# Optimization experiments

Hardware: AMD Instinct MI355X
Metric: run time of the kernel (lower is better)

The kernel has to match this reference:

```python
import jax, jax.numpy as jnp
import numpy as np

N = 50000      # nodes
F = 128        # num_features
E = 1600000    # edges
NHID = 256
J = 3          # orders
L = 3          # layers
G = 512        # graphs in batch
C = 10         # num_classes
NUM_DIFF = 13  # 1 + J + J^2


def setup_inputs() -> dict:
    key = jax.random.key(0)
    ks = jax.random.split(key, 32)
    rn = lambda k, shape, s=0.05: (jax.random.normal(k, shape, jnp.float32) * s)
    inp = {}
    inp["x"] = jax.random.normal(ks[0], (N, F), jnp.float32)
    inp["edge_index"] = jax.random.randint(ks[1], (2, E), 0, N)
    inp["diff_feat"] = jax.random.normal(ks[2], (NUM_DIFF, N, F), jnp.float32)
    inp["batch"] = jnp.sort(jax.random.randint(ks[3], (N,), 0, G))
    conv_in = [F, 2 * NHID, 2 * NHID]
    lin_in = [F * (J ** i) for i in range(L)]
    k = 4
    for i in range(L):
        inp[f"W_conv{i}"] = rn(ks[k], (conv_in[i], NHID)); k += 1
        inp[f"b_conv{i}"] = rn(ks[k], (NHID,)); k += 1
        inp[f"W_lin{i}"] = rn(ks[k], (lin_in[i], NHID)); k += 1
        inp[f"b_lin{i}"] = rn(ks[k], (NHID,)); k += 1
    bound = 1.0 / np.sqrt(J)
    inp["order_weights"] = jax.random.uniform(ks[k], (J,), jnp.float32, -bound, bound); k += 1
    inp["W_cls"] = rn(ks[k], (2 * NHID, NHID)); k += 1
    inp["b_cls"] = rn(ks[k], (NHID,)); k += 1
    inp["W_fc"] = rn(ks[k], (NHID, C)); k += 1
    inp["b_fc"] = rn(ks[k], (C,)); k += 1
    return inp


def _forward(x, diff_feat, order_weights, convW, convB, linW, linB,
             W_cls, b_cls, W_fc, b_fc, edge_index, batch):
    # GCNConv normalization with self-loops: D^-1/2 (A+I) D^-1/2
    loop = jnp.arange(N)
    src = jnp.concatenate([edge_index[0], loop])
    dst = jnp.concatenate([edge_index[1], loop])
    deg = jax.ops.segment_sum(jnp.ones((src.shape[0],), x.dtype), dst, num_segments=N)
    dinv = deg ** -0.5  # deg >= 1 due to self loops
    norm = (dinv[src] * dinv[dst])[:, None]

    def gcn(h, W, b):
        h = h @ W
        return jax.ops.segment_sum(h[src] * norm, dst, num_segments=N) + b

    comb = x
    begin = 0
    for i in range(L):
        convx = jax.nn.relu(gcn(comb, convW[i], convB[i]))  # dropout = identity (eval)
        count = J ** i
        lf = diff_feat[begin:begin + count]  # [count, N, F]
        if i > 0:
            ow = jnp.tile(order_weights, J ** (i - 1))[:, None, None]
            lf = ow * lf
        lf = jnp.moveaxis(lf, 0, 1).reshape(N, -1)  # [N, count*F]
        lin_sct = jax.nn.relu(lf @ linW[i] + linB[i])
        comb = jnp.concatenate([lin_sct, convx], axis=-1)  # [N, 2*NHID]
        begin += count
    convx = gcn(comb, W_cls, b_cls)  # no relu on final conv
    h_pooled = jax.ops.segment_sum(convx, batch, num_segments=G)  # global_add_pool
    return h_pooled @ W_fc + b_fc  # [G, C]


def reference(x, edge_index, diff_feat, batch,
              W_conv0, b_conv0, W_conv1, b_conv1, W_conv2, b_conv2,
              W_lin0, b_lin0, W_lin1, b_lin1, W_lin2, b_lin2,
              order_weights, W_cls, b_cls, W_fc, b_fc):
    convW = [W_conv0, W_conv1, W_conv2]
    convB = [b_conv0, b_conv1, b_conv2]
    linW = [W_lin0, W_lin1, W_lin2]
    linB = [b_lin0, b_lin1, b_lin2]
    return _forward(x, diff_feat, order_weights, convW, convB, linW, linB,
                    W_cls, b_cls, W_fc, b_fc, edge_index, batch)
```

## Files before the change

### kernel.cpp

```cpp
#include <hip/hip_runtime.h>

namespace {
constexpr int NN  = 50000;
constexpr int FF  = 128;
constexpr int EE  = 1600000;
constexpr int HID = 256;
constexpr int GG  = 512;
constexpr int CC  = 10;
}


__global__ __launch_bounds__(256) void k_zero_out(float* p, int n) {
    int i = blockIdx.x * 256 + threadIdx.x;
    if (i < n) p[i] = 0.0f;
}

__global__ __launch_bounds__(256) void k_fill_int(int* p, int val, int n) {
    int i = blockIdx.x * 256 + threadIdx.x;
    if (i < n) p[i] = val;
}

__global__ __launch_bounds__(256) void k_count(const int* __restrict__ dst,
                                               int* __restrict__ deg, int n) {
    int i = blockIdx.x * 256 + threadIdx.x;
    if (i < n) atomicAdd(&deg[dst[i]], 1);
}

__global__ __launch_bounds__(256) void k_dinv(const int* __restrict__ deg,
                                              float* __restrict__ dinv, int n) {
    int i = blockIdx.x * 256 + threadIdx.x;
    if (i < n) dinv[i] = 1.0f / sqrtf((float)deg[i]);
}

__global__ __launch_bounds__(256) void k_scan1(const int* __restrict__ deg,
                                               int* __restrict__ rowstart,
                                               int* __restrict__ bsum, int n) {
    __shared__ int s[256];
    int tid = threadIdx.x;
    int i = blockIdx.x * 256 + tid;
    int v = (i < n) ? (deg[i] - 1) : 0;
    s[tid] = v;
    __syncthreads();
    for (int off = 1; off < 256; off <<= 1) {
        int t = (tid >= off) ? s[tid - off] : 0;
        __syncthreads();
        s[tid] += t;
        __syncthreads();
    }
    if (i < n) rowstart[i] = s[tid] - v;
    if (tid == 255) bsum[blockIdx.x] = s[255];
}

__global__ __launch_bounds__(256) void k_scan2(int* __restrict__ bsum, int nb) {
    __shared__ int s[256];
    int tid = threadIdx.x;
    int v = (tid < nb) ? bsum[tid] : 0;
    s[tid] = v;
    __syncthreads();
    for (int off = 1; off < 256; off <<= 1) {
        int t = (tid >= off) ? s[tid - off] : 0;
        __syncthreads();
        s[tid] += t;
        __syncthreads();
    }
    if (tid < nb) bsum[tid] = s[tid] - v;
}

__global__ __launch_bounds__(256) void k_scan3(int* __restrict__ rowstart,
                                               const int* __restrict__ bsum,
                                               int n, int total) {
    int i = blockIdx.x * 256 + threadIdx.x;
    if (i < n) rowstart[i] += bsum[blockIdx.x];
    if (i == 0) rowstart[n] = total;
}

__global__ __launch_bounds__(256) void k_copy_int(const int* __restrict__ a,
                                                  int* __restrict__ b, int n) {
    int i = blockIdx.x * 256 + threadIdx.x;
    if (i < n) b[i] = a[i];
}

__global__ __launch_bounds__(256) void k_scatter(const int* __restrict__ srcs,
                                                 const int* __restrict__ dsts,
                                                 const float* __restrict__ dinv,
                                                 int* __restrict__ cursor,
                                                 int* __restrict__ csr_src,
                                                 float* __restrict__ csr_norm, int n) {
    int e = blockIdx.x * 256 + threadIdx.x;
    if (e < n) {
        int s = srcs[e], d = dsts[e];
        int pos = atomicAdd(&cursor[d], 1);
        csr_src[pos]  = s;
        csr_norm[pos] = dinv[s] * dinv[d];
    }
}

__global__ __launch_bounds__(256) void k_scale_wlin(const float* __restrict__ W,
                                                    const float* __restrict__ ow,
                                                    float* __restrict__ out, int total) {
    int i = blockIdx.x * 256 + threadIdx.x;
    if (i < total) {
        int row = i >> 8;
        out[i] = W[i] * ow[(row >> 7) % 3];
    }
}

__global__ __launch_bounds__(256) void k_gbounds(const int* __restrict__ batch,
                                                 int* __restrict__ gstart, int n, int g) {
    int i = blockIdx.x * 256 + threadIdx.x;
    if (i >= n) return;
    int b = batch[i];
    if (i == 0) {
        for (int q = 0; q <= b; ++q) gstart[q] = 0;
    } else {
        int bp = batch[i - 1];
        for (int q = bp + 1; q <= b; ++q) gstart[q] = i;
    }
    if (i == n - 1) {
        for (int q = b + 1; q <= g; ++q) gstart[q] = n;
    }
}

template <int VEC> struct VecT;
template <> struct VecT<4> { using T = float4; };
template <> struct VecT<2> { using T = float2; };

template <int VEC>
__global__ __launch_bounds__(256) void k_agg(const float* __restrict__ H,
                                             const int* __restrict__ rowstart,
                                             const int* __restrict__ csr_src,
                                             const float* __restrict__ csr_norm,
                                             const float* __restrict__ dinv,
                                             const float* __restrict__ bias,
                                             float* __restrict__ out,
                                             int out_stride, int out_off,
                                             int do_relu, int nN) {
    using VT = typename VecT<VEC>::T;
    constexpr int WIDTH = 64 * VEC;
    int n = (blockIdx.x * blockDim.x + threadIdx.x) >> 6;
    int lane = threadIdx.x & 63;
    if (n >= nN) return;

    float di = dinv[n];
    float selfw = di * di;
    float acc[VEC];
    {
        VT v = *reinterpret_cast<const VT*>(H + (size_t)n * WIDTH + lane * VEC);
        const float* vf = reinterpret_cast<const float*>(&v);
#pragma unroll
        for (int j = 0; j < VEC; ++j) acc[j] = vf[j] * selfw;
    }
    int s = rowstart[n], e = rowstart[n + 1];
    int i = s;
    for (; i + 3 < e; i += 4) {
        int s0 = csr_src[i], s1 = csr_src[i + 1], s2 = csr_src[i + 2], s3 = csr_src[i + 3];
        float w0 = csr_norm[i], w1 = csr_norm[i + 1], w2 = csr_norm[i + 2], w3 = csr_norm[i + 3];
        VT v0 = *reinterpret_cast<const VT*>(H + (size_t)s0 * WIDTH + lane * VEC);
        VT v1 = *reinterpret_cast<const VT*>(H + (size_t)s1 * WIDTH + lane * VEC);
        VT v2 = *reinterpret_cast<const VT*>(H + (size_t)s2 * WIDTH + lane * VEC);
        VT v3 = *reinterpret_cast<const VT*>(H + (size_t)s3 * WIDTH + lane * VEC);
        const float* f0 = reinterpret_cast<const float*>(&v0);
        const float* f1 = reinterpret_cast<const float*>(&v1);
        const float* f2 = reinterpret_cast<const float*>(&v2);
        const float* f3 = reinterpret_cast<const float*>(&v3);
#pragma unroll
        for (int j = 0; j < VEC; ++j)
            acc[j] += f0[j] * w0 + f1[j] * w1 + f2[j] * w2 + f3[j] * w3;
    }
    for (; i < e; ++i) {
        int ss = csr_src[i];
        float w = csr_norm[i];
        VT v = *reinterpret_cast<const VT*>(H + (size_t)ss * WIDTH + lane * VEC);
        const float* vf = reinterpret_cast<const float*>(&v);
#pragma unroll
        for (int j = 0; j < VEC; ++j) acc[j] += vf[j] * w;
    }
    if (bias) {
#pragma unroll
        for (int j = 0; j < VEC; ++j) acc[j] += bias[lane * VEC + j];
    }
    if (do_relu) {
#pragma unroll
        for (int j = 0; j < VEC; ++j) acc[j] = fmaxf(acc[j], 0.0f);
    }
    VT o;
    float* of = reinterpret_cast<float*>(&o);
#pragma unroll
    for (int j = 0; j < VEC; ++j) of[j] = acc[j];
    *reinterpret_cast<VT*>(out + (size_t)n * out_stride + out_off + lane * VEC) = o;
}

template <int LAYOUT>
__global__ __launch_bounds__(256) void k_gemm(const float* __restrict__ A, int ldaOrPlane,
                                              const float* __restrict__ W,
                                              const float* __restrict__ bias,
                                              float* __restrict__ out,
                                              int out_stride, int out_off,
                                              int nRows, int K, int do_relu) {
    __shared__ float As[16 * 132];
    __shared__ float Ws[16 * 64];
    int tid = threadIdx.x;
    int m0 = blockIdx.x * 128;
    int n0 = blockIdx.y * 64;
    int tx = tid & 15;
    int ty = tid >> 4;

    float acc[8][4];
#pragma unroll
    for (int i = 0; i < 8; ++i)
#pragma unroll
        for (int j = 0; j < 4; ++j) acc[i][j] = 0.0f;

    int nTiles = K >> 4;
    for (int t = 0; t < nTiles; ++t) {
        int k0 = t << 4;
        const float* Atile;
        int alda;
        if (LAYOUT == 0) {
            Atile = A + k0;
            alda = ldaOrPlane;
        } else {
            Atile = A + (size_t)(k0 >> 7) * ldaOrPlane + (k0 & 127);
            alda = 128;
        }
#pragma unroll
        for (int p = 0; p < 2; ++p) {
            int idx = tid + p * 256;
            int r = idx >> 2;
            int kk4 = idx & 3;
            float4 v = make_float4(0.f, 0.f, 0.f, 0.f);
            if (m0 + r < nRows)
                v = *reinterpret_cast<const float4*>(Atile + (size_t)(m0 + r) * alda + kk4 * 4);
            As[(kk4 * 4 + 0) * 132 + r] = v.x;
            As[(kk4 * 4 + 1) * 132 + r] = v.y;
            As[(kk4 * 4 + 2) * 132 + r] = v.z;
            As[(kk4 * 4 + 3) * 132 + r] = v.w;
        }
        {
            int kk = tid >> 4;
            int nn4 = tid & 15;
            float4 v = *reinterpret_cast<const float4*>(W + (size_t)(k0 + kk) * 256 + n0 + nn4 * 4);
            *reinterpret_cast<float4*>(Ws + kk * 64 + nn4 * 4) = v;
        }
        __syncthreads();
#pragma unroll
        for (int kk = 0; kk < 16; ++kk) {
            float4 a0 = *reinterpret_cast<const float4*>(As + kk * 132 + ty * 8);
            float4 a1 = *reinterpret_cast<const float4*>(As + kk * 132 + ty * 8 + 4);
            float4 w  = *reinterpret_cast<const float4*>(Ws + kk * 64 + tx * 4);
            float av[8] = {a0.x, a0.y, a0.z, a0.w, a1.x, a1.y, a1.z, a1.w};
            float wv[4] = {w.x, w.y, w.z, w.w};
#pragma unroll
            for (int i = 0; i < 8; ++i)
#pragma unroll
                for (int j = 0; j < 4; ++j) acc[i][j] += av[i] * wv[j];
        }
        __syncthreads();
    }
    float bv[4] = {0.f, 0.f, 0.f, 0.f};
    if (bias) {
#pragma unroll
        for (int j = 0; j < 4; ++j) bv[j] = bias[n0 + tx * 4 + j];
    }
#pragma unroll
    for (int i = 0; i < 8; ++i) {
        int gm = m0 + ty * 8 + i;
        if (gm < nRows) {
            float4 v;
            float r0 = acc[i][0] + bv[0];
            float r1 = acc[i][1] + bv[1];
            float r2 = acc[i][2] + bv[2];
            float r3 = acc[i][3] + bv[3];
            if (do_relu) {
                r0 = fmaxf(r0, 0.f); r1 = fmaxf(r1, 0.f);
                r2 = fmaxf(r2, 0.f); r3 = fmaxf(r3, 0.f);
            }
            v.x = r0; v.y = r1; v.z = r2; v.w = r3;
            *reinterpret_cast<float4*>(out + (size_t)gm * out_stride + out_off + n0 + tx * 4) = v;
        }
    }
}


__global__ __launch_bounds__(256) void k_pool(const float* __restrict__ Cfin,
                                              const int* __restrict__ gstart,
                                              float* __restrict__ pooled) {
    int g = blockIdx.x;
    int f = threadIdx.x;
    float acc = 0.0f;
    int s = gstart[g], e = gstart[g + 1];
    for (int n = s; n < e; ++n) acc += Cfin[(size_t)n * 512 + f];
    pooled[g * 256 + f] = acc;
}

__global__ __launch_bounds__(64) void k_fc(const float* __restrict__ pooled,
                                           const float* __restrict__ Wfc,
                                           const float* __restrict__ bfc,
                                           float* __restrict__ outp) {
    __shared__ float h[256];
    int g = blockIdx.x;
    for (int k = threadIdx.x; k < 256; k += 64) h[k] = pooled[g * 256 + k];
    __syncthreads();
    int c = threadIdx.x;
    if (c < CC) {
        float a = bfc[c];
        for (int k = 0; k < 256; ++k) a += h[k] * Wfc[k * CC + c];
        outp[g * CC + c] = a;
    }
}


extern "C" void kernel_launch(void* const* d_in, const int* in_sizes, int n_in,
                              void* d_out, int out_size, void* d_ws, size_t ws_size,
                              hipStream_t stream) {
    const float* x         = (const float*)d_in[0];
    const int*   edge      = (const int*)d_in[1];
    const float* diff_feat = (const float*)d_in[2];
    const int*   batch     = (const int*)d_in[3];
    const float* W_conv0 = (const float*)d_in[4];
    const float* b_conv0 = (const float*)d_in[5];
    const float* W_lin0  = (const float*)d_in[6];
    const float* b_lin0  = (const float*)d_in[7];
    const float* W_conv1 = (const float*)d_in[8];
    const float* b_conv1 = (const float*)d_in[9];
    const float* W_lin1  = (const float*)d_in[10];
    const float* b_lin1  = (const float*)d_in[11];
    const float* W_conv2 = (const float*)d_in[12];
    const float* b_conv2 = (const float*)d_in[13];
    const float* W_lin2  = (const float*)d_in[14];
    const float* b_lin2  = (const float*)d_in[15];
    const float* order_w = (const float*)d_in[16];
    const float* W_cls   = (const float*)d_in[17];
    const float* b_cls   = (const float*)d_in[18];
    const float* W_fc    = (const float*)d_in[19];
    const float* b_fc    = (const float*)d_in[20];
    float* outp = (float*)d_out;

    const int* esrc = edge;
    const int* edst = edge + EE;

    char* w = (char*)d_ws;
    size_t off = 0;
    auto alloc = [&](size_t bytes) {
        void* p = w + off;
        off = (off + bytes + 255) & ~(size_t)255;
        return p;
    };
    float* comb     = (float*)alloc((size_t)NN * 512 * 4);
    float* Bbuf     = (float*)alloc((size_t)NN * 256 * 4);
    float* Tbuf     = Bbuf;
    int*   csr_src  = (int*)alloc((size_t)EE * 4);
    float* csr_norm = (float*)alloc((size_t)EE * 4);
    int*   degi     = (int*)alloc((size_t)NN * 4);
    float* dinv     = (float*)alloc((size_t)NN * 4);
    int*   rowstart = (int*)alloc((size_t)(NN + 1) * 4);
    int*   cursor   = (int*)alloc((size_t)NN * 4);
    int*   bsum     = (int*)alloc(256 * 4);
    float* wlin1s   = (float*)alloc((size_t)384 * 256 * 4);
    float* wlin2s   = (float*)alloc((size_t)1152 * 256 * 4);
    int*   gstart   = (int*)alloc((size_t)(GG + 1) * 4);
    float* pooled   = (float*)alloc((size_t)GG * 256 * 4);
    (void)n_in; (void)in_sizes;

    if (ws_size < off) {
        k_zero_out<<<(out_size + 255) / 256, 256, 0, stream>>>(outp, out_size);
        return;
    }

    const int NB_N = (NN + 255) / 256;
    const int NB_E = (EE + 255) / 256;

    k_fill_int<<<NB_N, 256, 0, stream>>>(degi, 1, NN);
    k_count<<<NB_E, 256, 0, stream>>>(edst, degi, EE);
    k_dinv<<<NB_N, 256, 0, stream>>>(degi, dinv, NN);
    k_scan1<<<NB_N, 256, 0, stream>>>(degi, rowstart, bsum, NN);
    k_scan2<<<1, 256, 0, stream>>>(bsum, NB_N);
    k_scan3<<<NB_N, 256, 0, stream>>>(rowstart, bsum, NN, EE);
    k_copy_int<<<NB_N, 256, 0, stream>>>(rowstart, cursor, NN);
    k_scatter<<<NB_E, 256, 0, stream>>>(esrc, edst, dinv, cursor, csr_src, csr_norm, EE);
    k_scale_wlin<<<(384 * 256) / 256, 256, 0, stream>>>(W_lin1, order_w, wlin1s, 384 * 256);
    k_scale_wlin<<<(1152 * 256) / 256, 256, 0, stream>>>(W_lin2, order_w, wlin2s, 1152 * 256);
    k_gbounds<<<NB_N, 256, 0, stream>>>(batch, gstart, NN, GG);

    dim3 gemm_grid((NN + 127) / 128, 4);
    const int AGG_BLOCKS = (NN * 64 + 255) / 256;

    k_agg<2><<<AGG_BLOCKS, 256, 0, stream>>>(x, rowstart, csr_src, csr_norm, dinv,
                                             nullptr, Tbuf, 128, 0, 0, NN);
    k_gemm<0><<<gemm_grid, 256, 0, stream>>>(Tbuf, 128, W_conv0, b_conv0,
                                             comb, 512, 256, NN, 128, 1);
    k_gemm<0><<<gemm_grid, 256, 0, stream>>>(diff_feat, 128, W_lin0, b_lin0,
                                             comb, 512, 0, NN, 128, 1);

    k_gemm<0><<<gemm_grid, 256, 0, stream>>>(comb, 512, W_conv1, nullptr,
                                             Bbuf, 256, 0, NN, 512, 0);
    k_agg<4><<<AGG_BLOCKS, 256, 0, stream>>>(Bbuf, rowstart, csr_src, csr_norm, dinv,
                                             b_conv1, comb, 512, 256, 1, NN);
    k_gemm<1><<<gemm_grid, 256, 0, stream>>>(diff_feat + (size_t)NN * 128, NN * 128,
                                             wlin1s, b_lin1, comb, 512, 0, NN, 384, 1);

    k_gemm<0><<<gemm_grid, 256, 0, stream>>>(comb, 512, W_conv2, nullptr,
                                             Bbuf, 256, 0, NN, 512, 0);
    k_agg<4><<<AGG_BLOCKS, 256, 0, stream>>>(Bbuf, rowstart, csr_src, csr_norm, dinv,
                                             b_conv2, comb, 512, 256, 1, NN);
    k_gemm<1><<<gemm_grid, 256, 0, stream>>>(diff_feat + (size_t)4 * NN * 128, NN * 128,
                                             wlin2s, b_lin2, comb, 512, 0, NN, 1152, 1);

    k_gemm<0><<<gemm_grid, 256, 0, stream>>>(comb, 512, W_cls, nullptr,
                                             Bbuf, 256, 0, NN, 512, 0);
    k_agg<4><<<AGG_BLOCKS, 256, 0, stream>>>(Bbuf, rowstart, csr_src, csr_norm, dinv,
                                             b_cls, comb, 512, 0, 0, NN);

    k_pool<<<GG, 256, 0, stream>>>(comb, gstart, pooled);
    k_fc<<<GG, 64, 0, stream>>>(pooled, W_fc, b_fc, outp);
}
```

Baseline: 2.611 ms.

## Replace FP32 SIMT GEMMs with split-bf16 MFMA GEMMs and pre-transposed weights

All dense GEMMs move from a scalar FP32 register-tiled kernel to a matrix-core kernel using bf16 16x16x32 MFMA. To keep close to FP32 accuracy, each operand is split into high and low bf16 parts and three MFMA products are accumulated per tile. Weights are pre-split and transposed by a new prep kernel, which also folds in the order-weight scaling. Activations are split on the fly while loading into shared memory. Tiles grow to 128x128. The split adds conversion ALU work and roughly triples the matrix-core instruction count, and the epilogue now writes scalars instead of float4 stores.

```diff
diff --git a/kernel.cpp b/kernel.cpp
--- a/kernel.cpp
+++ b/kernel.cpp
@@ -2,11 +2,21 @@
 
 namespace {
 constexpr int NN  = 50000;
-constexpr int FF  = 128;
 constexpr int EE  = 1600000;
-constexpr int HID = 256;
 constexpr int GG  = 512;
 constexpr int CC  = 10;
+}
+
+typedef __attribute__((ext_vector_type(8))) short bf16x8;
+typedef __attribute__((ext_vector_type(4))) float f32x4;
+
+__device__ inline unsigned short bf16_rtn(float f) {
+    unsigned u = __float_as_uint(f);
+    unsigned r = (u + 0x7FFF + ((u >> 16) & 1)) >> 16;
+    return (unsigned short)r;
+}
+__device__ inline float bf16_to_f(unsigned short s) {
+    return __uint_as_float(((unsigned)s) << 16);
 }
 
 
@@ -95,14 +105,20 @@
     }
 }
 
-__global__ __launch_bounds__(256) void k_scale_wlin(const float* __restrict__ W,
-                                                    const float* __restrict__ ow,
-                                                    float* __restrict__ out, int total) {
-    int i = blockIdx.x * 256 + threadIdx.x;
-    if (i < total) {
-        int row = i >> 8;
-        out[i] = W[i] * ow[(row >> 7) % 3];
-    }
+__global__ __launch_bounds__(256) void k_prep_w(const float* __restrict__ W,
+                                                const float* __restrict__ ow,
+                                                int K, int useOw,
+                                                short* __restrict__ hi,
+                                                short* __restrict__ lo) {
+    int k = blockIdx.x * 256 + threadIdx.x;
+    int n = blockIdx.y;
+    if (k >= K) return;
+    float a = W[(size_t)k * 256 + n];
+    if (useOw) a *= ow[(k >> 7) % 3];
+    unsigned short h = bf16_rtn(a);
+    unsigned short l = bf16_rtn(a - bf16_to_f(h));
+    hi[(size_t)n * K + k] = (short)h;
+    lo[(size_t)n * K + k] = (short)l;
 }
 
 __global__ __launch_bounds__(256) void k_gbounds(const int* __restrict__ batch,
@@ -191,92 +207,115 @@
 }
 
 template <int LAYOUT>
-__global__ __launch_bounds__(256) void k_gemm(const float* __restrict__ A, int ldaOrPlane,
-                                              const float* __restrict__ W,
-                                              const float* __restrict__ bias,
-                                              float* __restrict__ out,
-                                              int out_stride, int out_off,
-                                              int nRows, int K, int do_relu) {
-    __shared__ float As[16 * 132];
-    __shared__ float Ws[16 * 64];
-    int tid = threadIdx.x;
-    int m0 = blockIdx.x * 128;
-    int n0 = blockIdx.y * 64;
-    int tx = tid & 15;
-    int ty = tid >> 4;
-
-    float acc[8][4];
-#pragma unroll
-    for (int i = 0; i < 8; ++i)
-#pragma unroll
-        for (int j = 0; j < 4; ++j) acc[i][j] = 0.0f;
-
-    int nTiles = K >> 4;
-    for (int t = 0; t < nTiles; ++t) {
-        int k0 = t << 4;
-        const float* Atile;
+__global__ __launch_bounds__(256) void k_gemm_mfma(
+    const float* __restrict__ A, int ldaOrPlane,
+    const short* __restrict__ Bh, const short* __restrict__ Bl,
+    const float* __restrict__ bias,
+    float* __restrict__ out, int out_stride, int out_off,
+    int nRows, int K, int do_relu)
+{
+    __shared__ short Ah[128 * 40];
+    __shared__ short Al[128 * 40];
+    __shared__ short Bhs[128 * 40];
+    __shared__ short Bls[128 * 40];
+
+    int tid  = threadIdx.x;
+    int m0   = blockIdx.x * 128;
+    int n0   = blockIdx.y * 128;
+    int lane = tid & 63;
+    int w    = tid >> 6;
+    int wr   = w >> 1, wc = w & 1;
+    int lrow = lane & 15;
+    int lkb  = lane >> 4;
+
+    f32x4 acc[4][4];
+#pragma unroll
+    for (int i = 0; i < 4; ++i)
+#pragma unroll
+        for (int j = 0; j < 4; ++j) {
+            acc[i][j].x = 0.f; acc[i][j].y = 0.f;
+            acc[i][j].z = 0.f; acc[i][j].w = 0.f;
+        }
+
+    int nSteps = K >> 5;
+    for (int kt = 0; kt < nSteps; ++kt) {
+        int k0 = kt << 5;
+        const float* Ag;
         int alda;
-        if (LAYOUT == 0) {
-            Atile = A + k0;
-            alda = ldaOrPlane;
-        } else {
-            Atile = A + (size_t)(k0 >> 7) * ldaOrPlane + (k0 & 127);
-            alda = 128;
-        }
-#pragma unroll
-        for (int p = 0; p < 2; ++p) {
-            int idx = tid + p * 256;
-            int r = idx >> 2;
-            int kk4 = idx & 3;
+        if (LAYOUT == 0) { Ag = A + k0; alda = ldaOrPlane; }
+        else { Ag = A + (size_t)(k0 >> 7) * ldaOrPlane + (k0 & 127); alda = 128; }
+
+#pragma unroll
+        for (int p = 0; p < 4; ++p) {
+            int idx = p * 256 + tid;
+            int r   = idx >> 3;
+            int kq  = idx & 7;
             float4 v = make_float4(0.f, 0.f, 0.f, 0.f);
             if (m0 + r < nRows)
-                v = *reinterpret_cast<const float4*>(Atile + (size_t)(m0 + r) * alda + kk4 * 4);
-            As[(kk4 * 4 + 0) * 132 + r] = v.x;
-            As[(kk4 * 4 + 1) * 132 + r] = v.y;
-            As[(kk4 * 4 + 2) * 132 + r] = v.z;
-            As[(kk4 * 4 + 3) * 132 + r] = v.w;
+                v = *reinterpret_cast<const float4*>(Ag + (size_t)(m0 + r) * alda + kq * 4);
+            unsigned short h0 = bf16_rtn(v.x), h1 = bf16_rtn(v.y),
+                           h2 = bf16_rtn(v.z), h3 = bf16_rtn(v.w);
+            unsigned short l0 = bf16_rtn(v.x - bf16_to_f(h0)),
+                           l1 = bf16_rtn(v.y - bf16_to_f(h1)),
+                           l2 = bf16_rtn(v.z - bf16_to_f(h2)),
+                           l3 = bf16_rtn(v.w - bf16_to_f(h3));
+            uint2 hp, lp;
+            hp.x = (unsigned)h0 | ((unsigned)h1 << 16);
+            hp.y = (unsigned)h2 | ((unsigned)h3 << 16);
+            lp.x = (unsigned)l0 | ((unsigned)l1 << 16);
+            lp.y = (unsigned)l2 | ((unsigned)l3 << 16);
+            *reinterpret_cast<uint2*>(&Ah[r * 40 + kq * 4]) = hp;
+            *reinterpret_cast<uint2*>(&Al[r * 40 + kq * 4]) = lp;
         }
-        {
-            int kk = tid >> 4;
-            int nn4 = tid & 15;
-            float4 v = *reinterpret_cast<const float4*>(W + (size_t)(k0 + kk) * 256 + n0 + nn4 * 4);
-            *reinterpret_cast<float4*>(Ws + kk * 64 + nn4 * 4) = v;
+#pragma unroll
+        for (int p = 0; p < 2; ++p) {
+            int idx = p * 256 + tid;
+            int n   = idx >> 2;
+            int kq  = idx & 3;
+            size_t g = (size_t)(n0 + n) * K + k0 + kq * 8;
+            *reinterpret_cast<bf16x8*>(&Bhs[n * 40 + kq * 8]) =
+                *reinterpret_cast<const bf16x8*>(&Bh[g]);
+            *reinterpret_cast<bf16x8*>(&Bls[n * 40 + kq * 8]) =
+                *reinterpret_cast<const bf16x8*>(&Bl[g]);
         }
         __syncthreads();
-#pragma unroll
-        for (int kk = 0; kk < 16; ++kk) {
-            float4 a0 = *reinterpret_cast<const float4*>(As + kk * 132 + ty * 8);
-            float4 a1 = *reinterpret_cast<const float4*>(As + kk * 132 + ty * 8 + 4);
-            float4 w  = *reinterpret_cast<const float4*>(Ws + kk * 64 + tx * 4);
-            float av[8] = {a0.x, a0.y, a0.z, a0.w, a1.x, a1.y, a1.z, a1.w};
-            float wv[4] = {w.x, w.y, w.z, w.w};
-#pragma unroll
-            for (int i = 0; i < 8; ++i)
-#pragma unroll
-                for (int j = 0; j < 4; ++j) acc[i][j] += av[i] * wv[j];
+
+        bf16x8 afh[4], afl[4], bfh[4], bfl[4];
+#pragma unroll
+        for (int f = 0; f < 4; ++f) {
+            int ar = wr * 64 + f * 16 + lrow;
+            afh[f] = *reinterpret_cast<const bf16x8*>(&Ah[ar * 40 + lkb * 8]);
+            afl[f] = *reinterpret_cast<const bf16x8*>(&Al[ar * 40 + lkb * 8]);
+            int br = wc * 64 + f * 16 + lrow;
+            bfh[f] = *reinterpret_cast<const bf16x8*>(&Bhs[br * 40 + lkb * 8]);
+            bfl[f] = *reinterpret_cast<const bf16x8*>(&Bls[br * 40 + lkb * 8]);
         }
-        __syncthreads();
-    }
-    float bv[4] = {0.f, 0.f, 0.f, 0.f};
-    if (bias) {
-#pragma unroll
-        for (int j = 0; j < 4; ++j) bv[j] = bias[n0 + tx * 4 + j];
-    }
-#pragma unroll
-    for (int i = 0; i < 8; ++i) {
-        int gm = m0 + ty * 8 + i;
-        if (gm < nRows) {
-            float4 v;
-            float r0 = acc[i][0] + bv[0];
-            float r1 = acc[i][1] + bv[1];
-            float r2 = acc[i][2] + bv[2];
-            float r3 = acc[i][3] + bv[3];
-            if (do_relu) {
-                r0 = fmaxf(r0, 0.f); r1 = fmaxf(r1, 0.f);
-                r2 = fmaxf(r2, 0.f); r3 = fmaxf(r3, 0.f);
+#pragma unroll
+        for (int i = 0; i < 4; ++i)
+#pragma unroll
+            for (int j = 0; j < 4; ++j) {
+                acc[i][j] = __builtin_amdgcn_mfma_f32_16x16x32_bf16(afh[i], bfh[j], acc[i][j], 0, 0, 0);
+                acc[i][j] = __builtin_amdgcn_mfma_f32_16x16x32_bf16(afh[i], bfl[j], acc[i][j], 0, 0, 0);
+                acc[i][j] = __builtin_amdgcn_mfma_f32_16x16x32_bf16(afl[i], bfh[j], acc[i][j], 0, 0, 0);
             }
-            v.x = r0; v.y = r1; v.z = r2; v.w = r3;
-            *reinterpret_cast<float4*>(out + (size_t)gm * out_stride + out_off + n0 + tx * 4) = v;
+        __syncthreads();
+    }
+
+#pragma unroll
+    for (int j = 0; j < 4; ++j) {
+        int col = n0 + wc * 64 + j * 16 + lrow;
+        float bv = bias ? bias[col] : 0.0f;
+#pragma unroll
+        for (int i = 0; i < 4; ++i) {
+#pragma unroll
+            for (int r = 0; r < 4; ++r) {
+                int m = m0 + wr * 64 + i * 16 + lkb * 4 + r;
+                if (m < nRows) {
+                    float v = acc[i][j][r] + bv;
+                    if (do_relu) v = fmaxf(v, 0.0f);
+                    out[(size_t)m * out_stride + out_off + col] = v;
+                }
+            }
         }
     }
 }
@@ -356,10 +395,22 @@
     int*   rowstart = (int*)alloc((size_t)(NN + 1) * 4);
     int*   cursor   = (int*)alloc((size_t)NN * 4);
     int*   bsum     = (int*)alloc(256 * 4);
-    float* wlin1s   = (float*)alloc((size_t)384 * 256 * 4);
-    float* wlin2s   = (float*)alloc((size_t)1152 * 256 * 4);
-    int*   gstart   = (int*)alloc((size_t)(GG + 1) * 4);
-    float* pooled   = (float*)alloc((size_t)GG * 256 * 4);
+    short* wt0h  = (short*)alloc((size_t)256 * 128 * 2);
+    short* wt0l  = (short*)alloc((size_t)256 * 128 * 2);
+    short* wl0h  = (short*)alloc((size_t)256 * 128 * 2);
+    short* wl0l  = (short*)alloc((size_t)256 * 128 * 2);
+    short* wt1h  = (short*)alloc((size_t)256 * 512 * 2);
+    short* wt1l  = (short*)alloc((size_t)256 * 512 * 2);
+    short* wl1h  = (short*)alloc((size_t)256 * 384 * 2);
+    short* wl1l  = (short*)alloc((size_t)256 * 384 * 2);
+    short* wt2h  = (short*)alloc((size_t)256 * 512 * 2);
+    short* wt2l  = (short*)alloc((size_t)256 * 512 * 2);
+    short* wl2h  = (short*)alloc((size_t)256 * 1152 * 2);
+    short* wl2l  = (short*)alloc((size_t)256 * 1152 * 2);
+    short* wch   = (short*)alloc((size_t)256 * 512 * 2);
+    short* wcl   = (short*)alloc((size_t)256 * 512 * 2);
+    int*   gstart = (int*)alloc((size_t)(GG + 1) * 4);
+    float* pooled = (float*)alloc((size_t)GG * 256 * 4);
     (void)n_in; (void)in_sizes;
 
     if (ws_size < off) {
@@ -378,36 +429,42 @@
     k_scan3<<<NB_N, 256, 0, stream>>>(rowstart, bsum, NN, EE);
     k_copy_int<<<NB_N, 256, 0, stream>>>(rowstart, cursor, NN);
     k_scatter<<<NB_E, 256, 0, stream>>>(esrc, edst, dinv, cursor, csr_src, csr_norm, EE);
-    k_scale_wlin<<<(384 * 256) / 256, 256, 0, stream>>>(W_lin1, order_w, wlin1s, 384 * 256);
-    k_scale_wlin<<<(1152 * 256) / 256, 256, 0, stream>>>(W_lin2, order_w, wlin2s, 1152 * 256);
     k_gbounds<<<NB_N, 256, 0, stream>>>(batch, gstart, NN, GG);
 
-    dim3 gemm_grid((NN + 127) / 128, 4);
+    k_prep_w<<<dim3(1, 256),  256, 0, stream>>>(W_conv0, order_w, 128,  0, wt0h, wt0l);
+    k_prep_w<<<dim3(1, 256),  256, 0, stream>>>(W_lin0,  order_w, 128,  0, wl0h, wl0l);
+    k_prep_w<<<dim3(2, 256),  256, 0, stream>>>(W_conv1, order_w, 512,  0, wt1h, wt1l);
+    k_prep_w<<<dim3(2, 256),  256, 0, stream>>>(W_lin1,  order_w, 384,  1, wl1h, wl1l);
+    k_prep_w<<<dim3(2, 256),  256, 0, stream>>>(W_conv2, order_w, 512,  0, wt2h, wt2l);
+    k_prep_w<<<dim3(5, 256),  256, 0, stream>>>(W_lin2,  order_w, 1152, 1, wl2h, wl2l);
+    k_prep_w<<<dim3(2, 256),  256, 0, stream>>>(W_cls,   order_w, 512,  0, wch,  wcl);
+
+    dim3 gg((NN + 127) / 128, 2);
     const int AGG_BLOCKS = (NN * 64 + 255) / 256;
 
     k_agg<2><<<AGG_BLOCKS, 256, 0, stream>>>(x, rowstart, csr_src, csr_norm, dinv,
                                              nullptr, Tbuf, 128, 0, 0, NN);
-    k_gemm<0><<<gemm_grid, 256, 0, stream>>>(Tbuf, 128, W_conv0, b_conv0,
-                                             comb, 512, 256, NN, 128, 1);
-    k_gemm<0><<<gemm_grid, 256, 0, stream>>>(diff_feat, 128, W_lin0, b_lin0,
-                                             comb, 512, 0, NN, 128, 1);
-
-    k_gemm<0><<<gemm_grid, 256, 0, stream>>>(comb, 512, W_conv1, nullptr,
-                                             Bbuf, 256, 0, NN, 512, 0);
+    k_gemm_mfma<0><<<gg, 256, 0, stream>>>(Tbuf, 128, wt0h, wt0l, b_conv0,
+                                           comb, 512, 256, NN, 128, 1);
+    k_gemm_mfma<0><<<gg, 256, 0, stream>>>(diff_feat, 128, wl0h, wl0l, b_lin0,
+                                           comb, 512, 0, NN, 128, 1);
+
+    k_gemm_mfma<0><<<gg, 256, 0, stream>>>(comb, 512, wt1h, wt1l, nullptr,
+                                           Bbuf, 256, 0, NN, 512, 0);
     k_agg<4><<<AGG_BLOCKS, 256, 0, stream>>>(Bbuf, rowstart, csr_src, csr_norm, dinv,
                                              b_conv1, comb, 512, 256, 1, NN);
-    k_gemm<1><<<gemm_grid, 256, 0, stream>>>(diff_feat + (size_t)NN * 128, NN * 128,
-                                             wlin1s, b_lin1, comb, 512, 0, NN, 384, 1);
-
-    k_gemm<0><<<gemm_grid, 256, 0, stream>>>(comb, 512, W_conv2, nullptr,
-                                             Bbuf, 256, 0, NN, 512, 0);
+    k_gemm_mfma<1><<<gg, 256, 0, stream>>>(diff_feat + (size_t)NN * 128, NN * 128,
+                                           wl1h, wl1l, b_lin1, comb, 512, 0, NN, 384, 1);
+
+    k_gemm_mfma<0><<<gg, 256, 0, stream>>>(comb, 512, wt2h, wt2l, nullptr,
+                                           Bbuf, 256, 0, NN, 512, 0);
     k_agg<4><<<AGG_BLOCKS, 256, 0, stream>>>(Bbuf, rowstart, csr_src, csr_norm, dinv,
                                              b_conv2, comb, 512, 256, 1, NN);
-    k_gemm<1><<<gemm_grid, 256, 0, stream>>>(diff_feat + (size_t)4 * NN * 128, NN * 128,
-                                             wlin2s, b_lin2, comb, 512, 0, NN, 1152, 1);
-
-    k_gemm<0><<<gemm_grid, 256, 0, stream>>>(comb, 512, W_cls, nullptr,
-                                             Bbuf, 256, 0, NN, 512, 0);
+    k_gemm_mfma<1><<<gg, 256, 0, stream>>>(diff_feat + (size_t)4 * NN * 128, NN * 128,
+                                           wl2h, wl2l, b_lin2, comb, 512, 0, NN, 1152, 1);
+
+    k_gemm_mfma<0><<<gg, 256, 0, stream>>>(comb, 512, wch, wcl, nullptr,
+                                           Bbuf, 256, 0, NN, 512, 0);
     k_agg<4><<<AGG_BLOCKS, 256, 0, stream>>>(Bbuf, rowstart, csr_src, csr_norm, dinv,
                                              b_cls, comb, 512, 0, 0, NN);
 
```

Result: faster. 2.167 ms (-17.0%).
